# Kernel optimization log

Hardware: AMD Instinct MI355X
Metric: run time of the kernel (lower is better)

The kernel has to match this reference:

```python
import jax, jax.numpy as jnp
import numpy as np

B, N, C = 1, 512, 64
CONTEXT = 3
HIDDEN = 256
N_OUT = 1
N_FEAT = C * 2 * CONTEXT  # join='cat' -> 2*C, then context shifts triple it
EPS = 1e-5


def pairing_cat(x_l, x_r, context):
    b, n, c = x_l.shape
    xl = jnp.broadcast_to(x_l[:, :, None, :], (b, n, n, c))
    xr = jnp.broadcast_to(x_r[:, None, :, :], (b, n, n, c))
    x = jnp.concatenate((xl, xr), axis=3)  # [B,N,N,2C]
    if context > 1:
        z = [x]
        for d in range(1, context // 2 + 1):
            z_u = jnp.zeros_like(x).at[:, d:, :-d, :].set(x[:, :-d, d:, :])
            z_d = jnp.zeros_like(x).at[:, :-d, d:, :].set(x[:, d:, :-d, :])
            z.append(z_u)
            z.append(z_d)
        x = jnp.concatenate(z, axis=3)  # [B,N,N,2C*context]
    return x


def setup_inputs() -> dict:
    key = jax.random.key(0)
    k = jax.random.split(key, 8)
    s1 = 1.0 / np.sqrt(N_FEAT)
    s2 = 1.0 / np.sqrt(HIDDEN)
    return {
        "x_l": jax.random.normal(k[0], (B, N, C), dtype=jnp.float32),
        "x_r": jax.random.normal(k[1], (B, N, C), dtype=jnp.float32),
        "W1": jax.random.uniform(k[2], (N_FEAT, HIDDEN), jnp.float32, -s1, s1),
        "b1": jax.random.uniform(k[3], (HIDDEN,), jnp.float32, -s1, s1),
        "gamma": jnp.ones((HIDDEN,), jnp.float32),
        "beta": jnp.zeros((HIDDEN,), jnp.float32),
        "W2": jax.random.uniform(k[4], (HIDDEN, N_OUT), jnp.float32, -s2, s2),
        "b2": jax.random.uniform(k[5], (N_OUT,), jnp.float32, -s2, s2),
    }


def reference(x_l, x_r, W1, b1, gamma, beta, W2, b2):
    x = pairing_cat(x_l, x_r, CONTEXT)  # [B,N,N,N_FEAT]
    h = jnp.einsum('bijf,fh->bijh', x, W1) + b1
    mu = jnp.mean(h, axis=-1, keepdims=True)
    var = jnp.mean(jnp.square(h - mu), axis=-1, keepdims=True)
    h = (h - mu) * jax.lax.rsqrt(var + EPS) * gamma + beta
    h = jax.nn.celu(h)  # dropout_rate=0.0 -> identity in eval/train
    y = jnp.einsum('bijh,ho->bijo', h, W2) + b2
    return y  # [B,N,N,1]
```

## Files before the change

kernel.cpp:

```cpp
#include <hip/hip_runtime.h>
#include <hip/hip_bf16.h>

#define NN  512
#define CC  64
#define HID 256
#define H4  (HID/4)
#define PSTRIDE (NN*HID)
#define PROWS 2
#define NB_BORDER 256

typedef short  bf16x8 __attribute__((ext_vector_type(8)));
typedef float  f32x4  __attribute__((ext_vector_type(4)));

__global__ __launch_bounds__(256) void proj_kernel(
    const float* __restrict__ xl, const float* __restrict__ xr,
    const float* __restrict__ W1, const float* __restrict__ b1,
    float* __restrict__ P)
{
  const int side = blockIdx.y;
  const int i0   = blockIdx.x * PROWS;
  const int h    = threadIdx.x;
  const float* __restrict__ x = side ? xr : xl;

  __shared__ float xs[PROWS][CC];
  if (threadIdx.x < PROWS * CC)
    xs[threadIdx.x >> 6][threadIdx.x & 63] = x[i0 * CC + threadIdx.x];
  __syncthreads();

  float acc0[PROWS], acc1[PROWS], acc2[PROWS];
#pragma unroll
  for (int r = 0; r < PROWS; r++) { acc0[r] = 0.f; acc1[r] = 0.f; acc2[r] = 0.f; }

  const int base = side ? CC : 0;
  const float* __restrict__ w0p = W1 + (base      ) * HID + h;
  const float* __restrict__ w1p = W1 + (base + 128) * HID + h;
  const float* __restrict__ w2p = W1 + (base + 256) * HID + h;
#pragma unroll 8
  for (int c = 0; c < CC; c++) {
    float w0 = w0p[c * HID];
    float w1 = w1p[c * HID];
    float w2 = w2p[c * HID];
#pragma unroll
    for (int r = 0; r < PROWS; r++) {
      float xv = xs[r][c];
      acc0[r] = fmaf(xv, w0, acc0[r]);
      acc1[r] = fmaf(xv, w1, acc1[r]);
      acc2[r] = fmaf(xv, w2, acc2[r]);
    }
  }

  float* __restrict__ O0 = P + (side ? 3 : 0) * PSTRIDE;
  float* __restrict__ O1 = P + (side ? 4 : 1) * PSTRIDE;
  float* __restrict__ O2 = P + (side ? 5 : 2) * PSTRIDE;
  const float bb = side ? 0.f : b1[h];
#pragma unroll
  for (int r = 0; r < PROWS; r++) {
    O0[(i0 + r) * HID + h] = acc0[r] + bb;
    O1[(i0 + r) * HID + h] = acc1[r];
    O2[(i0 + r) * HID + h] = acc2[r];
  }
}

__global__ __launch_bounds__(256) void prep_kernel(
    const float* __restrict__ P,
    float* __restrict__ Uf, float* __restrict__ Vf,
    unsigned short* __restrict__ Ubf, unsigned short* __restrict__ Vbf,
    float* __restrict__ rowstat)
{
  const int r = blockIdx.x, h = threadIdx.x;
  const float* __restrict__ PA = P;
  const float* __restrict__ PC = P + 1 * PSTRIDE;
  const float* __restrict__ PE = P + 2 * PSTRIDE;
  const float* __restrict__ PB = P + 3 * PSTRIDE;
  const float* __restrict__ PD = P + 4 * PSTRIDE;
  const float* __restrict__ PF = P + 5 * PSTRIDE;

  float u = PA[r * HID + h] + PC[(r - 1) * HID + h] + PE[(r + 1) * HID + h];
  float v = PB[r * HID + h] + PD[(r + 1) * HID + h] + PF[(r - 1) * HID + h];
  Uf[r * HID + h] = u;
  Vf[r * HID + h] = v;
  __hip_bfloat16 ub = __float2bfloat16(u), vb = __float2bfloat16(v);
  Ubf[r * HID + h] = *(unsigned short*)&ub;
  Vbf[r * HID + h] = *(unsigned short*)&vb;

  float u2 = u * u, v2 = v * v;
#pragma unroll
  for (int k = 32; k >= 1; k >>= 1) {
    u  += __shfl_xor(u,  k, 64);
    u2 += __shfl_xor(u2, k, 64);
    v  += __shfl_xor(v,  k, 64);
    v2 += __shfl_xor(v2, k, 64);
  }
  __shared__ float red[4][4];
  const int w = h >> 6;
  if ((h & 63) == 0) { red[w][0] = u; red[w][1] = u2; red[w][2] = v; red[w][3] = v2; }
  __syncthreads();
  if (h < 4)
    rowstat[h * NN + r] = red[0][h] + red[1][h] + red[2][h] + red[3][h];
}

__global__ __launch_bounds__(256) void cross_kernel(
    const unsigned short* __restrict__ Ubf,
    const unsigned short* __restrict__ Vbf,
    float* __restrict__ Cross)
{
  const int wave = threadIdx.x >> 6, lane = threadIdx.x & 63;
  const int t  = blockIdx.x * 4 + wave;
  const int ti = t >> 5, tj = t & 31;
  const int i0 = ti * 16, j0 = tj * 16;
  const int rc = lane & 15, kb = (lane >> 4) * 8;

  f32x4 acc = {0.f, 0.f, 0.f, 0.f};
#pragma unroll
  for (int k = 0; k < HID; k += 32) {
    bf16x8 a = *(const bf16x8*)(Ubf + (size_t)(i0 + rc) * HID + k + kb);
    bf16x8 b = *(const bf16x8*)(Vbf + (size_t)(j0 + rc) * HID + k + kb);
    acc = __builtin_amdgcn_mfma_f32_16x16x32_bf16(a, b, acc, 0, 0, 0);
  }
  const int orow = (lane >> 4) * 4, ocol = lane & 15;
#pragma unroll
  for (int r = 0; r < 4; r++)
    Cross[(size_t)(i0 + orow + r) * NN + j0 + ocol] = acc[r];
}

__device__ __forceinline__ float celu1(float x) {
  float e = __expf(x) - 1.f;
  return x > 0.f ? x : e;
}

__global__ __launch_bounds__(256) void pair_kernel(
    const float* __restrict__ P,
    const float* __restrict__ Uf, const float* __restrict__ Vf,
    const float* __restrict__ Cross, const float* __restrict__ rowstat,
    const float* __restrict__ gamma, const float* __restrict__ beta,
    const float* __restrict__ W2, const float* __restrict__ b2,
    float* __restrict__ out)
{
  const int wave = threadIdx.x >> 6, lane = threadIdx.x & 63;
  const float b2s = b2[0];

  if (blockIdx.x >= NB_BORDER) {
    const int bx    = blockIdx.x - NB_BORDER;
    const int i     = 1 + (bx >> 2);
    const int chunk = bx & 3;
    const int g = lane >> 4, q = lane & 15;

    const float4* U4 = (const float4*)(Uf + i * HID + q * 16);
    const float4 u0 = U4[0], u1 = U4[1], u2 = U4[2], u3 = U4[3];
    const float4* G4 = (const float4*)(gamma + q * 16);
    const float4 ga0 = G4[0], ga1 = G4[1], ga2 = G4[2], ga3 = G4[3];
    const float4* B4 = (const float4*)(beta + q * 16);
    const float4 bt0 = B4[0], bt1 = B4[1], bt2 = B4[2], bt3 = B4[3];
    const float4* W4 = (const float4*)(W2 + q * 16);
    const float4 w0 = W4[0], w1 = W4[1], w2 = W4[2], w3 = W4[3];

    const float sUi  = rowstat[0 * NN + i];
    const float sU2i = rowstat[1 * NN + i];
    const float* __restrict__ sV  = rowstat + 2 * NN;
    const float* __restrict__ sV2 = rowstat + 3 * NN;

    const int jbase = 1 + chunk * 128 + wave * 32 + g;
#pragma unroll 2
    for (int m = 0; m < 8; m++) {
      const int j  = jbase + m * 4;
      const int jc = j <= 510 ? j : 510;
      const float4* V4 = (const float4*)(Vf + jc * HID + q * 16);
      const float4 v0 = V4[0], v1 = V4[1], v2 = V4[2], v3 = V4[3];
      const float Cr = Cross[i * NN + jc];
      const float mu = (sUi + sV[jc]) * (1.f / HID);
      const float t  = fmaf(2.f, Cr, sU2i + sV2[jc]) * (1.f / HID);
      const float rs = rsqrtf(t - mu * mu + 1e-5f);
      const float mrs = -mu * rs;

      auto doh = [&](float& acc, float U, float V, float G, float Bt, float W) {
        float s = U + V;
        float n = fmaf(fmaf(s, rs, mrs), G, Bt);
        acc = fmaf(celu1(n), W, acc);
      };
      float r0 = 0.f, r1 = 0.f, r2 = 0.f, r3 = 0.f;
      doh(r0, u0.x, v0.x, ga0.x, bt0.x, w0.x);
      doh(r0, u0.y, v0.y, ga0.y, bt0.y, w0.y);
      doh(r0, u0.z, v0.z, ga0.z, bt0.z, w0.z);
      doh(r0, u0.w, v0.w, ga0.w, bt0.w, w0.w);
      doh(r1, u1.x, v1.x, ga1.x, bt1.x, w1.x);
      doh(r1, u1.y, v1.y, ga1.y, bt1.y, w1.y);
      doh(r1, u1.z, v1.z, ga1.z, bt1.z, w1.z);
      doh(r1, u1.w, v1.w, ga1.w, bt1.w, w1.w);
      doh(r2, u2.x, v2.x, ga2.x, bt2.x, w2.x);
      doh(r2, u2.y, v2.y, ga2.y, bt2.y, w2.y);
      doh(r2, u2.z, v2.z, ga2.z, bt2.z, w2.z);
      doh(r2, u2.w, v2.w, ga2.w, bt2.w, w2.w);
      doh(r3, u3.x, v3.x, ga3.x, bt3.x, w3.x);
      doh(r3, u3.y, v3.y, ga3.y, bt3.y, w3.y);
      doh(r3, u3.z, v3.z, ga3.z, bt3.z, w3.z);
      doh(r3, u3.w, v3.w, ga3.w, bt3.w, w3.w);
      float racc = (r0 + r1) + (r2 + r3);

#pragma unroll
      for (int k = 1; k <= 8; k <<= 1)
        racc += __shfl_xor(racc, k, 64);
      if (q == 0 && j <= 510)
        out[i * NN + j] = racc + b2s;
    }
  } else {
    const int gw = blockIdx.x * 4 + wave;
    const float4* P4 = (const float4*)P;
    const float4* PA = P4 + 0 * (PSTRIDE / 4);
    const float4* PC = P4 + 1 * (PSTRIDE / 4);
    const float4* PE = P4 + 2 * (PSTRIDE / 4);
    const float4* PB = P4 + 3 * (PSTRIDE / 4);
    const float4* PD = P4 + 4 * (PSTRIDE / 4);
    const float4* PF = P4 + 5 * (PSTRIDE / 4);
    const float4 g  = ((const float4*)gamma)[lane];
    const float4 be = ((const float4*)beta)[lane];
    const float4 w2 = ((const float4*)W2)[lane];

#pragma unroll
    for (int tt = 0; tt < 2; tt++) {
      const int p = gw * 2 + tt;
      if (p >= 2044) break;
      int i, j;
      if      (p < 512)  { i = 0;        j = p;        }
      else if (p < 1024) { i = 511;      j = p - 512;  }
      else if (p < 1534) { i = p - 1023; j = 0;        }
      else               { i = p - 1533; j = 511;      }

      const float4 a  = PA[i * H4 + lane];
      const float4 cu = PC[(i - 1) * H4 + lane];
      const float4 ed = PE[(i + 1) * H4 + lane];
      const float4 b  = PB[j * H4 + lane];
      const float4 du = PD[(j + 1) * H4 + lane];
      const float4 fd = PF[(j - 1) * H4 + lane];
      const float mu_m = (i >= 1 && j <= NN - 2) ? 1.f : 0.f;
      const float md_m = (i <= NN - 2 && j >= 1) ? 1.f : 0.f;

      float s0 = fmaf(md_m, ed.x + fd.x, fmaf(mu_m, cu.x + du.x, a.x + b.x));
      float s1 = fmaf(md_m, ed.y + fd.y, fmaf(mu_m, cu.y + du.y, a.y + b.y));
      float s2 = fmaf(md_m, ed.z + fd.z, fmaf(mu_m, cu.z + du.z, a.z + b.z));
      float s3 = fmaf(md_m, ed.w + fd.w, fmaf(mu_m, cu.w + du.w, a.w + b.w));

      float sum = (s0 + s1) + (s2 + s3);
      float ssq = fmaf(s0, s0, fmaf(s1, s1, fmaf(s2, s2, s3 * s3)));
#pragma unroll
      for (int off = 32; off >= 1; off >>= 1) {
        sum += __shfl_xor(sum, off, 64);
        ssq += __shfl_xor(ssq, off, 64);
      }
      const float mu  = sum * (1.f / HID);
      const float var = fmaf(ssq, 1.f / HID, -mu * mu);
      const float rs  = rsqrtf(var + 1e-5f);
      const float mrs = -mu * rs;

      auto nrm = [&](float s, float G, float Bt) {
        return fmaf(fmaf(s, rs, mrs), G, Bt);
      };
      float racc = fmaf(celu1(nrm(s0, g.x, be.x)), w2.x,
                   fmaf(celu1(nrm(s1, g.y, be.y)), w2.y,
                   fmaf(celu1(nrm(s2, g.z, be.z)), w2.z,
                        celu1(nrm(s3, g.w, be.w)) * w2.w)));
#pragma unroll
      for (int off = 32; off >= 1; off >>= 1)
        racc += __shfl_xor(racc, off, 64);
      if (lane == 0) out[i * NN + j] = racc + b2s;
    }
  }
}

extern "C" void kernel_launch(void* const* d_in, const int* in_sizes, int n_in,
                              void* d_out, int out_size, void* d_ws, size_t ws_size,
                              hipStream_t stream)
{
  const float* xl    = (const float*)d_in[0];
  const float* xr    = (const float*)d_in[1];
  const float* W1    = (const float*)d_in[2];
  const float* b1    = (const float*)d_in[3];
  const float* gamma = (const float*)d_in[4];
  const float* beta  = (const float*)d_in[5];
  const float* W2    = (const float*)d_in[6];
  const float* b2    = (const float*)d_in[7];
  float* out = (float*)d_out;

  float* P     = (float*)d_ws;
  float* Uf    = P + 6 * PSTRIDE;
  float* Vf    = Uf + NN * HID;
  float* Cross = Vf + NN * HID;
  unsigned short* Ubf = (unsigned short*)(Cross + NN * NN);
  unsigned short* Vbf = Ubf + NN * HID;
  float* rowstat = (float*)(Vbf + NN * HID);

  proj_kernel<<<dim3(NN / PROWS, 2), 256, 0, stream>>>(xl, xr, W1, b1, P);
  prep_kernel<<<NN, 256, 0, stream>>>(P, Uf, Vf, Ubf, Vbf, rowstat);
  cross_kernel<<<256, 256, 0, stream>>>(Ubf, Vbf, Cross);
  pair_kernel<<<NB_BORDER + 2040, 256, 0, stream>>>(P, Uf, Vf, Cross, rowstat,
                                                    gamma, beta, W2, b2, out);
}
```

Before: 112.5 us.

## Transpose V layout and map one pair per thread in interior pair kernel

```diff
diff --git a/kernel.cpp b/kernel.cpp
--- a/kernel.cpp
+++ b/kernel.cpp
@@ -63,7 +63,7 @@
 
 __global__ __launch_bounds__(256) void prep_kernel(
     const float* __restrict__ P,
-    float* __restrict__ Uf, float* __restrict__ Vf,
+    float* __restrict__ Uf, float* __restrict__ Vt,
     unsigned short* __restrict__ Ubf, unsigned short* __restrict__ Vbf,
     float* __restrict__ rowstat)
 {
@@ -78,7 +78,7 @@
   float u = PA[r * HID + h] + PC[(r - 1) * HID + h] + PE[(r + 1) * HID + h];
   float v = PB[r * HID + h] + PD[(r + 1) * HID + h] + PF[(r - 1) * HID + h];
   Uf[r * HID + h] = u;
-  Vf[r * HID + h] = v;
+  Vt[((h >> 2) * NN + r) * 4 + (h & 3)] = v;
   __hip_bfloat16 ub = __float2bfloat16(u), vb = __float2bfloat16(v);
   Ubf[r * HID + h] = *(unsigned short*)&ub;
   Vbf[r * HID + h] = *(unsigned short*)&vb;
@@ -130,7 +130,7 @@
 
 __global__ __launch_bounds__(256) void pair_kernel(
     const float* __restrict__ P,
-    const float* __restrict__ Uf, const float* __restrict__ Vf,
+    const float* __restrict__ Uf, const float* __restrict__ Vt,
     const float* __restrict__ Cross, const float* __restrict__ rowstat,
     const float* __restrict__ gamma, const float* __restrict__ beta,
     const float* __restrict__ W2, const float* __restrict__ b2,
@@ -140,68 +140,40 @@
   const float b2s = b2[0];
 
   if (blockIdx.x >= NB_BORDER) {
-    const int bx    = blockIdx.x - NB_BORDER;
-    const int i     = 1 + (bx >> 2);
-    const int chunk = bx & 3;
-    const int g = lane >> 4, q = lane & 15;
-
-    const float4* U4 = (const float4*)(Uf + i * HID + q * 16);
-    const float4 u0 = U4[0], u1 = U4[1], u2 = U4[2], u3 = U4[3];
-    const float4* G4 = (const float4*)(gamma + q * 16);
-    const float4 ga0 = G4[0], ga1 = G4[1], ga2 = G4[2], ga3 = G4[3];
-    const float4* B4 = (const float4*)(beta + q * 16);
-    const float4 bt0 = B4[0], bt1 = B4[1], bt2 = B4[2], bt3 = B4[3];
-    const float4* W4 = (const float4*)(W2 + q * 16);
-    const float4 w0 = W4[0], w1 = W4[1], w2 = W4[2], w3 = W4[3];
-
-    const float sUi  = rowstat[0 * NN + i];
-    const float sU2i = rowstat[1 * NN + i];
-    const float* __restrict__ sV  = rowstat + 2 * NN;
-    const float* __restrict__ sV2 = rowstat + 3 * NN;
-
-    const int jbase = 1 + chunk * 128 + wave * 32 + g;
-#pragma unroll 2
-    for (int m = 0; m < 8; m++) {
-      const int j  = jbase + m * 4;
-      const int jc = j <= 510 ? j : 510;
-      const float4* V4 = (const float4*)(Vf + jc * HID + q * 16);
-      const float4 v0 = V4[0], v1 = V4[1], v2 = V4[2], v3 = V4[3];
-      const float Cr = Cross[i * NN + jc];
-      const float mu = (sUi + sV[jc]) * (1.f / HID);
-      const float t  = fmaf(2.f, Cr, sU2i + sV2[jc]) * (1.f / HID);
-      const float rs = rsqrtf(t - mu * mu + 1e-5f);
-      const float mrs = -mu * rs;
-
-      auto doh = [&](float& acc, float U, float V, float G, float Bt, float W) {
-        float s = U + V;
-        float n = fmaf(fmaf(s, rs, mrs), G, Bt);
-        acc = fmaf(celu1(n), W, acc);
-      };
-      float r0 = 0.f, r1 = 0.f, r2 = 0.f, r3 = 0.f;
-      doh(r0, u0.x, v0.x, ga0.x, bt0.x, w0.x);
-      doh(r0, u0.y, v0.y, ga0.y, bt0.y, w0.y);
-      doh(r0, u0.z, v0.z, ga0.z, bt0.z, w0.z);
-      doh(r0, u0.w, v0.w, ga0.w, bt0.w, w0.w);
-      doh(r1, u1.x, v1.x, ga1.x, bt1.x, w1.x);
-      doh(r1, u1.y, v1.y, ga1.y, bt1.y, w1.y);
-      doh(r1, u1.z, v1.z, ga1.z, bt1.z, w1.z);
-      doh(r1, u1.w, v1.w, ga1.w, bt1.w, w1.w);
-      doh(r2, u2.x, v2.x, ga2.x, bt2.x, w2.x);
-      doh(r2, u2.y, v2.y, ga2.y, bt2.y, w2.y);
-      doh(r2, u2.z, v2.z, ga2.z, bt2.z, w2.z);
-      doh(r2, u2.w, v2.w, ga2.w, bt2.w, w2.w);
-      doh(r3, u3.x, v3.x, ga3.x, bt3.x, w3.x);
-      doh(r3, u3.y, v3.y, ga3.y, bt3.y, w3.y);
-      doh(r3, u3.z, v3.z, ga3.z, bt3.z, w3.z);
-      doh(r3, u3.w, v3.w, ga3.w, bt3.w, w3.w);
-      float racc = (r0 + r1) + (r2 + r3);
-
-#pragma unroll
-      for (int k = 1; k <= 8; k <<= 1)
-        racc += __shfl_xor(racc, k, 64);
-      if (q == 0 && j <= 510)
-        out[i * NN + j] = racc + b2s;
+    const int bx = blockIdx.x - NB_BORDER;
+    const int i  = 1 + (bx >> 1);
+    const int jj = ((bx & 1) << 8) + threadIdx.x;
+    const int j  = jj < 1 ? 1 : (jj > 510 ? 510 : jj);
+
+    __shared__ float4 K4s[HID];
+    K4s[threadIdx.x] = make_float4(gamma[threadIdx.x], beta[threadIdx.x],
+                                   W2[threadIdx.x], Uf[i * HID + threadIdx.x]);
+    __syncthreads();
+
+    const float mu  = (rowstat[0 * NN + i] + rowstat[2 * NN + j]) * (1.f / HID);
+    const float tq  = fmaf(2.f, Cross[i * NN + j],
+                           rowstat[1 * NN + i] + rowstat[3 * NN + j]) * (1.f / HID);
+    const float rs  = rsqrtf(tq - mu * mu + 1e-5f);
+    const float mrs = -mu * rs;
+
+    float racc0 = 0.f, racc1 = 0.f;
+    const float4* __restrict__ Vp = (const float4*)Vt;
+#pragma unroll 4
+    for (int hb = 0; hb < H4; hb++) {
+      const float4 v4 = Vp[hb * NN + j];
+      const float vv[4] = {v4.x, v4.y, v4.z, v4.w};
+#pragma unroll
+      for (int q = 0; q < 4; q++) {
+        const float4 K = K4s[hb * 4 + q];
+        const float s = vv[q] + K.w;
+        const float n = fmaf(fmaf(s, rs, mrs), K.x, K.y);
+        const float c = celu1(n);
+        if (q & 1) racc1 = fmaf(c, K.z, racc1);
+        else       racc0 = fmaf(c, K.z, racc0);
+      }
     }
+    if (jj >= 1 && jj <= 510)
+      out[i * NN + jj] = racc0 + racc1 + b2s;
   } else {
     const int gw = blockIdx.x * 4 + wave;
     const float4* P4 = (const float4*)P;
@@ -282,15 +254,15 @@
 
   float* P     = (float*)d_ws;
   float* Uf    = P + 6 * PSTRIDE;
-  float* Vf    = Uf + NN * HID;
-  float* Cross = Vf + NN * HID;
+  float* Vt    = Uf + NN * HID;
+  float* Cross = Vt + NN * HID;
   unsigned short* Ubf = (unsigned short*)(Cross + NN * NN);
   unsigned short* Vbf = Ubf + NN * HID;
   float* rowstat = (float*)(Vbf + NN * HID);
 
   proj_kernel<<<dim3(NN / PROWS, 2), 256, 0, stream>>>(xl, xr, W1, b1, P);
-  prep_kernel<<<NN, 256, 0, stream>>>(P, Uf, Vf, Ubf, Vbf, rowstat);
+  prep_kernel<<<NN, 256, 0, stream>>>(P, Uf, Vt, Ubf, Vbf, rowstat);
   cross_kernel<<<256, 256, 0, stream>>>(Ubf, Vbf, Cross);
-  pair_kernel<<<NB_BORDER + 2040, 256, 0, stream>>>(P, Uf, Vf, Cross, rowstat,
+  pair_kernel<<<NB_BORDER + 1020, 256, 0, stream>>>(P, Uf, Vt, Cross, rowstat,
                                                     gamma, beta, W2, b2, out);
 }
```

New measurement: 108.1 us. 3.9% less time.
